# Kernel optimization log

Hardware: AMD Instinct MI355X
Metric: run time of the kernel (lower is better)

The kernel has to match this reference:

```python
import jax, jax.numpy as jnp
from jax import lax
import numpy as np

B, T, D, H = 64, 2048, 256, 256


def setup_inputs() -> dict:
    key = jax.random.key(0)
    k1, k2, k3 = jax.random.split(key, 3)
    s_x = 1.0 / np.sqrt(D)
    s_h = 1.0 / np.sqrt(H)
    return {
        "inputs": jax.random.normal(k1, (B, T, D), dtype=jnp.float32),
        "hidden": jnp.zeros((1, B, H), dtype=jnp.float32),
        "Wx": jax.random.normal(k2, (3 * H, D), dtype=jnp.float32) * s_x,
        "bx": jnp.zeros((3 * H,), dtype=jnp.float32),
        "Wh": jax.random.normal(k3, (3 * H, H), dtype=jnp.float32) * s_h,
        "bh": jnp.zeros((3 * H,), dtype=jnp.float32),
    }


def reference(inputs, hidden, Wx, bx, Wh, bh):
    # inputs: [B, T, D]; hidden: [1, B, H] (leading 1 broadcast, as in the torch code)
    def step(h, x_t):
        # x_t: [B, 3H] (precomputed x2h); h: [1, B, H]
        h_t = h[0] @ Wh.T + bh                      # [B, 3H] (h2h + squeeze)
        x_r, x_u, x_n = jnp.split(x_t, 3, axis=1)
        h_r, h_u, h_n = jnp.split(h_t, 3, axis=1)
        reset = jax.nn.sigmoid(x_r + h_r)
        upd = jax.nn.sigmoid(x_u + h_u)
        new = jnp.tanh(x_n + reset * h_n)
        hy = upd * h + (1.0 - upd) * new            # broadcasts to [1, B, H]
        return hy, hy[0]

    # Hoist the input projection out of the scan (same math, one big GEMM).
    xs = jnp.einsum('btd,gd->btg', inputs, Wx) + bx  # [B, T, 3H]
    xs = jnp.transpose(xs, (1, 0, 2))                # [T, B, 3H]
    _, hs = lax.scan(step, hidden, xs)               # hs: [T, B, H]
    return jnp.transpose(hs, (1, 0, 2))              # [B, T, H]
```

## Files before the change

### kernel.cpp

```cpp
#include <hip/hip_runtime.h>
#include <hip/hip_fp16.h>

#define B_SZ 64
#define T_SZ 2048
#define D_SZ 256
#define H_SZ 256
#define G3   768
#define M_SZ (B_SZ * T_SZ)

typedef _Float16 half2v __attribute__((ext_vector_type(2)));
typedef _Float16 half4v __attribute__((ext_vector_type(4)));
typedef _Float16 half8v __attribute__((ext_vector_type(8)));
typedef float    f32x4  __attribute__((ext_vector_type(4)));

static __device__ __forceinline__ float fdot2f(uint a, uint b, float acc) {
#if __has_builtin(__builtin_amdgcn_fdot2)
  return __builtin_amdgcn_fdot2(__builtin_bit_cast(half2v, a),
                                __builtin_bit_cast(half2v, b), acc, false);
#else
  half2v av = __builtin_bit_cast(half2v, a), bv = __builtin_bit_cast(half2v, b);
  acc = fmaf((float)av[0], (float)bv[0], acc);
  acc = fmaf((float)av[1], (float)bv[1], acc);
  return acc;
#endif
}

static __device__ __forceinline__ float h2f(ushort u) {
  return (float)__builtin_bit_cast(_Float16, u);
}
static __device__ __forceinline__ ushort f2h(float x) {
  return __builtin_bit_cast(ushort, (_Float16)x);
}
static __device__ __forceinline__ float fast_rcp(float x) {
  return __builtin_amdgcn_rcpf(x);
}

__global__ void prep_wx(const float* __restrict__ Wx, ushort* __restrict__ Wxh) {
  int i = blockIdx.x * 256 + threadIdx.x;
  if (i < G3 * D_SZ) Wxh[i] = f2h(Wx[i]);
}

__global__ void prep_wq(const float* __restrict__ Wh, uint* __restrict__ Wq) {
  int f = blockIdx.x * 256 + threadIdx.x;
  int e = f & 3;
  int t2 = f >> 2;
  int j = t2 % G3;
  int s4 = t2 / G3;
  int kp = 4 * s4 + e;
  float a = Wh[(size_t)j * D_SZ + 2 * kp];
  float b = Wh[(size_t)j * D_SZ + 2 * kp + 1];
  Wq[f] = (uint)f2h(a) | ((uint)f2h(b) << 16);
}

__global__ __launch_bounds__(256) void gemm_x(
    const float* __restrict__ A,
    const ushort* __restrict__ Bw,
    const float* __restrict__ bx,
    ushort* __restrict__ xs) {
  __shared__ _Float16 As[128][72];
  __shared__ _Float16 Bs[256][72];
  const int nt = blockIdx.x, mt = blockIdx.y;
  const int tid = threadIdx.x;
  const int lane = tid & 63, wv = tid >> 6;
  const int wr = (wv >> 1) * 64, wc = (wv & 1) * 128;
  const int l15 = lane & 15, l4 = lane >> 4;
  f32x4 acc[4][8] = {};
  for (int kt = 0; kt < 4; kt++) {
#pragma unroll
    for (int i = 0; i < 8; i++) {
      int f = tid + i * 256;
      int r = f >> 4, c4 = f & 15;
      float4 v = *(const float4*)(A + (size_t)(mt * 128 + r) * D_SZ + kt * 64 + c4 * 4);
      half4v h;
      h[0] = (_Float16)v.x; h[1] = (_Float16)v.y;
      h[2] = (_Float16)v.z; h[3] = (_Float16)v.w;
      *(half4v*)&As[r][c4 * 4] = h;
    }
#pragma unroll
    for (int i = 0; i < 8; i++) {
      int f = tid + i * 256;
      int r = f >> 3, c8 = f & 7;
      uint4 v = *(const uint4*)(Bw + (size_t)(nt * 256 + r) * D_SZ + kt * 64 + c8 * 8);
      *(uint4*)&Bs[r][c8 * 8] = v;
    }
    __syncthreads();
#pragma unroll
    for (int kk = 0; kk < 2; kk++) {
      half8v af[4], bf[8];
#pragma unroll
      for (int m = 0; m < 4; m++)
        af[m] = *(const half8v*)&As[wr + m * 16 + l15][kk * 32 + l4 * 8];
#pragma unroll
      for (int n = 0; n < 8; n++)
        bf[n] = *(const half8v*)&Bs[wc + n * 16 + l15][kk * 32 + l4 * 8];
#pragma unroll
      for (int m = 0; m < 4; m++) {
#pragma unroll
        for (int n = 0; n < 8; n++) {
          acc[m][n] = __builtin_amdgcn_mfma_f32_16x16x32_f16(af[m], bf[n], acc[m][n], 0, 0, 0);
        }
      }
    }
    __syncthreads();
  }
#pragma unroll
  for (int n = 0; n < 8; n++) {
    int col = nt * 256 + wc + n * 16 + l15;
    float bxv = bx[col];
#pragma unroll
    for (int m = 0; m < 4; m++) {
#pragma unroll
      for (int v4 = 0; v4 < 4; v4++) {
        int row = mt * 128 + wr + m * 16 + l4 * 4 + v4;
        xs[(size_t)row * G3 + col] = f2h(acc[m][n][v4] + bxv);
      }
    }
  }
}

__global__ __launch_bounds__(768, 3) void gru_rec(
    const ushort* __restrict__ xs,
    const uint* __restrict__ Wq,
    const float* __restrict__ bh,
    const float* __restrict__ hid,
    float* __restrict__ out) {
  const int b = blockIdx.x;
  const int j = threadIdx.x;
  __shared__ alignas(16) ushort h16[H_SZ];
  __shared__ float rs[H_SZ];
  __shared__ float us[H_SZ];

  uint4 w4[32];
  {
    const uint4* wp = (const uint4*)Wq;
#pragma unroll
    for (int s4 = 0; s4 < 32; s4++) w4[s4] = wp[(size_t)s4 * G3 + j];
  }
  const float bhj = bh[j];
  if (j < H_SZ) h16[j] = f2h(hid[b * H_SZ + j]);
  __syncthreads();

  const ushort* xrow = xs + (size_t)b * T_SZ * G3 + j;
  float* orow = out + (size_t)b * T_SZ * H_SZ;
  ushort xu = xrow[0];

#pragma unroll 1
  for (int t = 0; t < T_SZ; t++) {
    ushort xnext = (t + 1 < T_SZ) ? xrow[(size_t)(t + 1) * G3] : (ushort)0;
    float x = h2f(xu);

    float d0 = 0.f, d1 = 0.f, d2 = 0.f, d3 = 0.f;
    const uint4* hq = (const uint4*)h16;
#pragma unroll
    for (int c = 0; c < 32; c++) {
      uint4 q = hq[c];
      uint4 wv = w4[c];
      d0 = fdot2f(wv.x, q.x, d0);
      d1 = fdot2f(wv.y, q.y, d1);
      d2 = fdot2f(wv.z, q.z, d2);
      d3 = fdot2f(wv.w, q.w, d3);
    }
    float pre = ((d0 + d1) + (d2 + d3)) + bhj;

    if (j < 512) {
      float a = pre + x;
      float s = fast_rcp(1.f + __expf(-a));
      if (j < H_SZ) rs[j] = s;
      else          us[j - H_SZ] = s;
    }
    asm volatile("s_waitcnt lgkmcnt(0)" ::: "memory");
    __builtin_amdgcn_s_barrier();

    if (j >= 512) {
      int i = j - 512;
      float r = rs[i], u = us[i];
      float hold = h2f(h16[i]);
      float arg = x + r * pre;
      float e = __expf(-2.f * fabsf(arg));
      float th = copysignf((1.f - e) * fast_rcp(1.f + e), arg);
      float hn = u * hold + (1.f - u) * th;
      orow[(size_t)t * H_SZ + i] = hn;
      h16[i] = f2h(hn);
    }
    asm volatile("s_waitcnt lgkmcnt(0)" ::: "memory");
    __builtin_amdgcn_s_barrier();
    xu = xnext;
  }
}

extern "C" void kernel_launch(void* const* d_in, const int* in_sizes, int n_in,
                              void* d_out, int out_size, void* d_ws, size_t ws_size,
                              hipStream_t stream) {
  const float* inp = (const float*)d_in[0];
  const float* hid = (const float*)d_in[1];
  const float* Wx  = (const float*)d_in[2];
  const float* bx  = (const float*)d_in[3];
  const float* Wh  = (const float*)d_in[4];
  const float* bh  = (const float*)d_in[5];
  float* out = (float*)d_out;

  char* ws = (char*)d_ws;
  ushort* xs = (ushort*)ws;
  size_t xs_bytes = (size_t)M_SZ * G3 * sizeof(ushort);
  ushort* Wxh = (ushort*)(ws + xs_bytes);
  uint* Wq = (uint*)(ws + xs_bytes + (size_t)G3 * D_SZ * sizeof(ushort));

  prep_wx<<<768, 256, 0, stream>>>(Wx, Wxh);
  prep_wq<<<384, 256, 0, stream>>>(Wh, Wq);
  gemm_x<<<dim3(3, 1024), 256, 0, stream>>>(inp, Wxh, bx, xs);
  gru_rec<<<B_SZ, G3, 0, stream>>>(xs, Wq, bh, hid, out);
}
```

Measured before the change: 2.509 ms.

## Batch eight sequences per block and compute recurrent GEMM with MFMA

The recurrent kernel now handles eight batch rows per 256-thread block. The h2h product runs as 16x16x32 MFMA tiles, with the weights pre-swizzled into register-resident B fragments. The precomputed input projection is stored time-major with the r/u hidden biases folded in, and each step's slice is prefetched into double-buffered shared memory. Hidden state is double-buffered so each step needs one barrier instead of two. The trade-off is only 8 blocks on the GPU and heavy register pressure from 96 uint4 weight fragments per thread.

After: 4.405 ms. 75.6% more time.

```diff
diff --git a/kernel.cpp b/kernel.cpp
--- a/kernel.cpp
+++ b/kernel.cpp
@@ -7,24 +7,13 @@
 #define H_SZ 256
 #define G3   768
 #define M_SZ (B_SZ * T_SZ)
-
-typedef _Float16 half2v __attribute__((ext_vector_type(2)));
+#define NB   8
+#define HP   264
+
 typedef _Float16 half4v __attribute__((ext_vector_type(4)));
 typedef _Float16 half8v __attribute__((ext_vector_type(8)));
 typedef float    f32x4  __attribute__((ext_vector_type(4)));
 
-static __device__ __forceinline__ float fdot2f(uint a, uint b, float acc) {
-#if __has_builtin(__builtin_amdgcn_fdot2)
-  return __builtin_amdgcn_fdot2(__builtin_bit_cast(half2v, a),
-                                __builtin_bit_cast(half2v, b), acc, false);
-#else
-  half2v av = __builtin_bit_cast(half2v, a), bv = __builtin_bit_cast(half2v, b);
-  acc = fmaf((float)av[0], (float)bv[0], acc);
-  acc = fmaf((float)av[1], (float)bv[1], acc);
-  return acc;
-#endif
-}
-
 static __device__ __forceinline__ float h2f(ushort u) {
   return (float)__builtin_bit_cast(_Float16, u);
 }
@@ -40,23 +29,27 @@
   if (i < G3 * D_SZ) Wxh[i] = f2h(Wx[i]);
 }
 
-__global__ void prep_wq(const float* __restrict__ Wh, uint* __restrict__ Wq) {
-  int f = blockIdx.x * 256 + threadIdx.x;
-  int e = f & 3;
-  int t2 = f >> 2;
-  int j = t2 % G3;
-  int s4 = t2 / G3;
-  int kp = 4 * s4 + e;
-  float a = Wh[(size_t)j * D_SZ + 2 * kp];
-  float b = Wh[(size_t)j * D_SZ + 2 * kp + 1];
-  Wq[f] = (uint)f2h(a) | ((uint)f2h(b) << 16);
+__global__ void prep_wb(const float* __restrict__ Wh, uint* __restrict__ Wb) {
+  int F = blockIdx.x * 256 + threadIdx.x;
+  int d = F & 3;
+  int l = (F >> 2) & 63;
+  int ks = (F >> 8) & 7;
+  int ctf = F >> 11;
+  int w = ctf / 12, rem = ctf % 12;
+  int gate = rem >> 2, i = rem & 3;
+  int col = gate * 256 + (4 * w + i) * 16 + (l & 15);
+  int k0 = ks * 32 + (l >> 4) * 8 + 2 * d;
+  float a = Wh[(size_t)col * D_SZ + k0];
+  float b = Wh[(size_t)col * D_SZ + k0 + 1];
+  Wb[F] = (uint)f2h(a) | ((uint)f2h(b) << 16);
 }
 
 __global__ __launch_bounds__(256) void gemm_x(
     const float* __restrict__ A,
     const ushort* __restrict__ Bw,
     const float* __restrict__ bx,
-    ushort* __restrict__ xs) {
+    const float* __restrict__ bh,
+    ushort* __restrict__ xs2) {
   __shared__ _Float16 As[128][72];
   __shared__ _Float16 Bs[256][72];
   const int nt = blockIdx.x, mt = blockIdx.y;
@@ -106,85 +99,136 @@
 #pragma unroll
   for (int n = 0; n < 8; n++) {
     int col = nt * 256 + wc + n * 16 + l15;
-    float bxv = bx[col];
+    float bias = bx[col] + (col < 512 ? bh[col] : 0.f);
 #pragma unroll
     for (int m = 0; m < 4; m++) {
 #pragma unroll
       for (int v4 = 0; v4 < 4; v4++) {
         int row = mt * 128 + wr + m * 16 + l4 * 4 + v4;
-        xs[(size_t)row * G3 + col] = f2h(acc[m][n][v4] + bxv);
-      }
-    }
-  }
-}
-
-__global__ __launch_bounds__(768, 3) void gru_rec(
-    const ushort* __restrict__ xs,
-    const uint* __restrict__ Wq,
+        int bb = row >> 11, tt = row & 2047;
+        xs2[((size_t)tt * 64 + bb) * G3 + col] = f2h(acc[m][n][v4] + bias);
+      }
+    }
+  }
+}
+
+__global__ __launch_bounds__(256, 1) void gru_rec(
+    const ushort* __restrict__ xs2,
+    const uint* __restrict__ Wb,
     const float* __restrict__ bh,
     const float* __restrict__ hid,
     float* __restrict__ out) {
-  const int b = blockIdx.x;
-  const int j = threadIdx.x;
-  __shared__ alignas(16) ushort h16[H_SZ];
-  __shared__ float rs[H_SZ];
-  __shared__ float us[H_SZ];
-
-  uint4 w4[32];
+  const int b0 = blockIdx.x * NB;
+  const int tid = threadIdx.x;
+  const int l = tid & 63, w = tid >> 6;
+  const int l15 = l & 15;
+
+  __shared__ ushort hbuf[2][16][HP];
+  __shared__ ushort xbuf[2][NB * G3];
+
+  uint4 Bf[12][8];
   {
-    const uint4* wp = (const uint4*)Wq;
-#pragma unroll
-    for (int s4 = 0; s4 < 32; s4++) w4[s4] = wp[(size_t)s4 * G3 + j];
-  }
-  const float bhj = bh[j];
-  if (j < H_SZ) h16[j] = f2h(hid[b * H_SZ + j]);
+    const uint4* wb = (const uint4*)Wb;
+#pragma unroll
+    for (int ct = 0; ct < 12; ct++)
+#pragma unroll
+      for (int ks = 0; ks < 8; ks++)
+        Bf[ct][ks] = wb[(size_t)((w * 12 + ct) * 8 + ks) * 64 + l];
+  }
+
+  const int qd = l >> 4;
+  const int bbase = (qd & 1) * 4 + (qd & 2);
+
+  float bhn[4], hreg[4][2];
+#pragma unroll
+  for (int i = 0; i < 4; i++) {
+    int unit = (4 * w + i) * 16 + l15;
+    bhn[i] = bh[512 + unit];
+#pragma unroll
+    for (int be = 0; be < 2; be++)
+      hreg[i][be] = hid[(b0 + bbase + be) * H_SZ + unit];
+  }
+
+  {
+    uint* hz = (uint*)hbuf;
+    for (int idx = tid; idx < 2 * 16 * HP / 2; idx += 256) hz[idx] = 0u;
+  }
   __syncthreads();
-
-  const ushort* xrow = xs + (size_t)b * T_SZ * G3 + j;
-  float* orow = out + (size_t)b * T_SZ * H_SZ;
-  ushort xu = xrow[0];
+  for (int idx = tid; idx < NB * H_SZ; idx += 256) {
+    int bb = idx >> 8, u = idx & 255;
+    hbuf[0][bb][u] = f2h(hid[(b0 + bb) * H_SZ + u]);
+  }
+  {
+    const uint4* gx = (const uint4*)(xs2 + (size_t)b0 * G3);
+    uint4* xb = (uint4*)xbuf[0];
+    xb[tid] = gx[tid]; xb[tid + 256] = gx[tid + 256]; xb[tid + 512] = gx[tid + 512];
+  }
+  __syncthreads();
 
 #pragma unroll 1
   for (int t = 0; t < T_SZ; t++) {
-    ushort xnext = (t + 1 < T_SZ) ? xrow[(size_t)(t + 1) * G3] : (ushort)0;
-    float x = h2f(xu);
-
-    float d0 = 0.f, d1 = 0.f, d2 = 0.f, d3 = 0.f;
-    const uint4* hq = (const uint4*)h16;
-#pragma unroll
-    for (int c = 0; c < 32; c++) {
-      uint4 q = hq[c];
-      uint4 wv = w4[c];
-      d0 = fdot2f(wv.x, q.x, d0);
-      d1 = fdot2f(wv.y, q.y, d1);
-      d2 = fdot2f(wv.z, q.z, d2);
-      d3 = fdot2f(wv.w, q.w, d3);
-    }
-    float pre = ((d0 + d1) + (d2 + d3)) + bhj;
-
-    if (j < 512) {
-      float a = pre + x;
-      float s = fast_rcp(1.f + __expf(-a));
-      if (j < H_SZ) rs[j] = s;
-      else          us[j - H_SZ] = s;
+    const int cur = t & 1, nxt = cur ^ 1;
+
+    int tn = (t + 1 < T_SZ) ? t + 1 : t;
+    const uint4* gx = (const uint4*)(xs2 + ((size_t)tn * 64 + b0) * G3);
+    uint4 xg0 = gx[tid], xg1 = gx[tid + 256], xg2 = gx[tid + 512];
+
+    f32x4 acc[12];
+    half8v Af[8];
+    const ushort* hrow = &hbuf[cur][l15][(l >> 4) * 8];
+#pragma unroll
+    for (int ks = 0; ks < 3; ks++)
+      Af[ks] = __builtin_bit_cast(half8v, *(const uint4*)(hrow + ks * 32));
+#pragma unroll
+    for (int ct = 0; ct < 12; ct++)
+      acc[ct] = __builtin_amdgcn_mfma_f32_16x16x32_f16(
+          Af[0], __builtin_bit_cast(half8v, Bf[ct][0]),
+          (f32x4){0.f, 0.f, 0.f, 0.f}, 0, 0, 0);
+#pragma unroll
+    for (int ks = 1; ks < 8; ks++) {
+      if (ks + 2 < 8)
+        Af[ks + 2] = __builtin_bit_cast(half8v, *(const uint4*)(hrow + (ks + 2) * 32));
+#pragma unroll
+      for (int ct = 0; ct < 12; ct++)
+        acc[ct] = __builtin_amdgcn_mfma_f32_16x16x32_f16(
+            Af[ks], __builtin_bit_cast(half8v, Bf[ct][ks]), acc[ct], 0, 0, 0);
+    }
+
+#pragma unroll
+    for (int i = 0; i < 4; i++) {
+      int unit = (4 * w + i) * 16 + l15;
+      float v[3][2];
+#pragma unroll
+      for (int g = 0; g < 3; g++) {
+        f32x4 a = acc[g * 4 + i];
+        float s2 = __shfl_xor(a[2], 32);
+        float s3 = __shfl_xor(a[3], 32);
+        v[g][0] = (l < 32) ? a[0] : s2;
+        v[g][1] = (l < 32) ? a[1] : s3;
+      }
+#pragma unroll
+      for (int be = 0; be < 2; be++) {
+        int bb = bbase + be;
+        const ushort* xp = &xbuf[cur][bb * G3 + unit];
+        float xr = h2f(xp[0]), xu = h2f(xp[256]), xn = h2f(xp[512]);
+        float rr = fast_rcp(1.f + __expf(-(xr + v[0][be])));
+        float uu = fast_rcp(1.f + __expf(-(xu + v[1][be])));
+        float arg = xn + rr * (v[2][be] + bhn[i]);
+        float e2 = __expf(-2.f * fabsf(arg));
+        float th = copysignf((1.f - e2) * fast_rcp(1.f + e2), arg);
+        float hn = th + uu * (hreg[i][be] - th);
+        hreg[i][be] = hn;
+        out[((size_t)(b0 + bb) * T_SZ + t) * H_SZ + unit] = hn;
+        hbuf[nxt][bb][unit] = f2h(hn);
+      }
+    }
+
+    {
+      uint4* xb = (uint4*)xbuf[nxt];
+      xb[tid] = xg0; xb[tid + 256] = xg1; xb[tid + 512] = xg2;
     }
     asm volatile("s_waitcnt lgkmcnt(0)" ::: "memory");
     __builtin_amdgcn_s_barrier();
-
-    if (j >= 512) {
-      int i = j - 512;
-      float r = rs[i], u = us[i];
-      float hold = h2f(h16[i]);
-      float arg = x + r * pre;
-      float e = __expf(-2.f * fabsf(arg));
-      float th = copysignf((1.f - e) * fast_rcp(1.f + e), arg);
-      float hn = u * hold + (1.f - u) * th;
-      orow[(size_t)t * H_SZ + i] = hn;
-      h16[i] = f2h(hn);
-    }
-    asm volatile("s_waitcnt lgkmcnt(0)" ::: "memory");
-    __builtin_amdgcn_s_barrier();
-    xu = xnext;
   }
 }
 
@@ -200,13 +244,13 @@
   float* out = (float*)d_out;
 
   char* ws = (char*)d_ws;
-  ushort* xs = (ushort*)ws;
+  ushort* xs2 = (ushort*)ws;
   size_t xs_bytes = (size_t)M_SZ * G3 * sizeof(ushort);
   ushort* Wxh = (ushort*)(ws + xs_bytes);
-  uint* Wq = (uint*)(ws + xs_bytes + (size_t)G3 * D_SZ * sizeof(ushort));
+  uint* Wb = (uint*)(ws + xs_bytes + (size_t)G3 * D_SZ * sizeof(ushort));
 
   prep_wx<<<768, 256, 0, stream>>>(Wx, Wxh);
-  prep_wq<<<384, 256, 0, stream>>>(Wh, Wq);
-  gemm_x<<<dim3(3, 1024), 256, 0, stream>>>(inp, Wxh, bx, xs);
-  gru_rec<<<B_SZ, G3, 0, stream>>>(xs, Wq, bh, hid, out);
-}
+  prep_wb<<<384, 256, 0, stream>>>(Wh, Wb);
+  gemm_x<<<dim3(3, 1024), 256, 0, stream>>>(inp, Wxh, bx, bh, xs2);
+  gru_rec<<<B_SZ / NB, 256, 0, stream>>>(xs2, Wb, bh, hid, out);
+}
```
